# Performance work log

Hardware: AMD Instinct MI355X
Metric: run time of the kernel (lower is better)

Reference implementation:

```python
import jax, jax.numpy as jnp
import numpy as np

N_NODES = 20000
N_EDGES = 240000
N_GRAPHS = 200
D_IN = 118
H = 256          # simplified hidden width standing in for the mul=50 irreps hidden
NB = 10          # number_of_basis
RH = 100         # fc_neurons hidden
L = 3            # layers
SH = 9           # lmax=2 -> 1+3+5 spherical-harmonic channels
MAX_RADIUS = 5.0
NUM_NEIGHBORS = 12.0


def setup_inputs() -> dict:
    key = jax.random.key(0)
    ks = jax.random.split(key, 16)
    inp = {
        "x": jax.random.normal(ks[0], (N_NODES, D_IN), jnp.float32),
        "pos": jax.random.normal(ks[1], (N_NODES, 3), jnp.float32),
        "edge_shift": jax.random.normal(ks[2], (N_EDGES, 3), jnp.float32),
        "lattice": jax.random.normal(ks[3], (N_GRAPHS, 3, 3), jnp.float32),
        "W_embed": jax.random.normal(ks[4], (D_IN, H), jnp.float32) / np.sqrt(D_IN),
        "r1": jax.random.normal(ks[5], (L, NB, RH), jnp.float32) / np.sqrt(NB),
        "b1": jax.random.normal(ks[6], (L, RH), jnp.float32) * 0.1,
        "r2": jax.random.normal(ks[7], (L, RH, H), jnp.float32) / np.sqrt(RH),
        "Wtp": jax.random.normal(ks[8], (L, SH, H, H), jnp.float32) / np.sqrt(SH * H),
        "Wself": jax.random.normal(ks[9], (L, H, H), jnp.float32) / np.sqrt(H),
        "Wskip": jax.random.normal(ks[10], (L, H, H), jnp.float32) / np.sqrt(H),
        "Wout": jax.random.normal(ks[11], (H, 1), jnp.float32) / np.sqrt(H),
        "edge_index": jax.random.randint(ks[12], (2, N_EDGES), 0, N_NODES, jnp.int64)
                        if jax.config.jax_enable_x64 else
                      jax.random.randint(ks[12], (2, N_EDGES), 0, N_NODES).astype(jnp.int32),
        "batch": jnp.sort(jax.random.randint(ks[13], (N_NODES,), 0, N_GRAPHS)).astype(jnp.int32),
    }
    return inp


def _sph_harm_lmax2(u):
    """Component-normalized real spherical harmonics up to l=2 on unit vectors u [E,3]."""
    x, y, z = u[:, 0], u[:, 1], u[:, 2]
    c1 = np.sqrt(3.0)
    c2 = np.sqrt(15.0)
    return jnp.stack([
        jnp.ones_like(x),                       # l=0
        c1 * x, c1 * y, c1 * z,                 # l=1
        c2 * x * y, c2 * y * z,                 # l=2
        (np.sqrt(5.0) / 2.0) * (3.0 * z * z - 1.0),
        c2 * x * z, (c2 / 2.0) * (x * x - y * y),
    ], axis=1)                                  # [E, 9]


def _soft_one_hot_cosine(lens):
    """e3nn soft_one_hot_linspace(basis='cosine', cutoff=True) * sqrt(NB)."""
    vals = jnp.linspace(0.0, MAX_RADIUS, NB + 2)
    step = vals[1] - vals[0]
    vals = vals[1:-1]
    diff = (lens[:, None] - vals[None, :]) / step          # [E, NB]
    emb = jnp.cos(0.5 * jnp.pi * diff) * (diff > -1.0) * (diff < 1.0)
    return emb * np.sqrt(float(NB))


def _forward(x, pos, edge_shift, lattice, W_embed, r1, b1, r2, Wtp, Wself, Wskip, Wout,
             edge_src, edge_dst, batch):
    edge_batch = batch[edge_src]                            # [E]
    # periodic edge vectors: pos[dst] - pos[src] + shift @ lattice[graph]
    edge_vec = pos[edge_dst] - pos[edge_src] + jnp.einsum(
        'ni,nij->nj', edge_shift, lattice[edge_batch])      # [E, 3]
    lens = jnp.linalg.norm(edge_vec, axis=1)                # [E]
    u = edge_vec / (lens[:, None] + 1e-12)
    sh = _sph_harm_lmax2(u)                                 # [E, 9]
    emb = _soft_one_hot_cosine(lens)                        # [E, NB]

    h = x @ W_embed                                         # [N, H]
    inv_sqrt_deg = 1.0 / np.sqrt(NUM_NEIGHBORS)
    for l in range(L):
        radial = jax.nn.silu(emb @ r1[l] + b1[l]) @ r2[l]   # [E, H]
        hs = h[edge_src] * radial                           # gather + radial gate
        # weighted tensor-product-like message: sum_a (hs * sh_a) @ Wtp[l, a]
        msg = (hs * sh[:, 0:1]) @ Wtp[l, 0]
        for a in range(1, SH):
            msg = msg + (hs * sh[:, a:a + 1]) @ Wtp[l, a]   # [E, H]
        agg = jax.ops.segment_sum(msg, edge_dst, num_segments=N_NODES) * inv_sqrt_deg
        h = jax.nn.gelu(agg @ Wself[l] + h @ Wskip[l])      # [N, H]

    node_out = h @ Wout                                     # [N, 1]
    # scatter_mean over graphs
    sums = jax.ops.segment_sum(node_out, batch, num_segments=N_GRAPHS)
    cnts = jax.ops.segment_sum(jnp.ones((N_NODES, 1), node_out.dtype), batch,
                               num_segments=N_GRAPHS)
    return sums / jnp.maximum(cnts, 1.0)                    # [G, 1]


def reference(x, pos, edge_shift, lattice, W_embed, r1, b1, r2, Wtp, Wself, Wskip, Wout,
              edge_index, batch):
    return _forward(x, pos, edge_shift, lattice, W_embed, r1, b1, r2, Wtp, Wself, Wskip,
                    Wout, edge_index[0], edge_index[1], batch)
```

## Files before the change

### kernel.cpp

```cpp
#include <hip/hip_runtime.h>
#include <hip/hip_bf16.h>
#include <cstddef>
#include <cstdint>

#define NNODE  20000
#define MPAD   20096
#define NEDGE  240000
#define NGRAPH 200
#define DIN    118
#define HD     256
#define NBASIS 10
#define RHID   100
#define NLAYER 3
#define NSH    9
#define SHSTR  16
#define KTP    (NSH * HD)
#define KTOT   (KTP + HD)
#define KR2    128
#define KEMB   128
#define SPLITK 4
#define KCH    (KTOT / SPLITK)
#define NRT    (MPAD / 64)

typedef _Float16 f16;
typedef _Float16 f16x2 __attribute__((ext_vector_type(2)));
typedef _Float16 f16x4 __attribute__((ext_vector_type(4)));
typedef _Float16 f16x8 __attribute__((ext_vector_type(8)));
typedef float    f32x4 __attribute__((ext_vector_type(4)));

__device__ __forceinline__ float gelu_tanh(float v) {
  float v3 = v * v * v;
  return 0.5f * v * (1.f + tanhf(0.7978845608028654f * (v + 0.044715f * v3)));
}

__device__ __forceinline__ int perm64(int rho) {
  return (rho & ~63) | ((rho & 15) * 4 + ((rho >> 4) & 3));
}
__device__ __forceinline__ int inv_perm64(int n) {
  return (n & ~63) | (((n & 3) << 4) | ((n >> 2) & 15));
}

__global__ void deg_hist_kernel(const int* __restrict__ ei, int* __restrict__ deg)
{
  int e = blockIdx.x * 256 + threadIdx.x;
  if (e >= NEDGE) return;
  atomicAdd(&deg[ei[NEDGE + e]], 1);
}

__global__ void scan_kernel(const int* __restrict__ deg, int* __restrict__ rowptr)
{
  __shared__ int part[256];
  int t = threadIdx.x;
  const int chunk = (NNODE + 255) / 256;
  int start = t * chunk;
  int end = min(start + chunk, NNODE);
  int s = 0;
  for (int i = start; i < end; ++i) s += deg[i];
  part[t] = s;
  __syncthreads();
  for (int off = 1; off < 256; off <<= 1) {
    int v = (t >= off) ? part[t - off] : 0;
    __syncthreads();
    part[t] += v;
    __syncthreads();
  }
  int run = (t == 0) ? 0 : part[t - 1];
  for (int i = start; i < end; ++i) { rowptr[i] = run; run += deg[i]; }
  if (t == 255) rowptr[NNODE] = run;
}

__global__ void edge_geom_kernel(const float* __restrict__ pos,
                                 const float* __restrict__ shift,
                                 const float* __restrict__ lat,
                                 const int* __restrict__ ei,
                                 const int* __restrict__ batch,
                                 const int* __restrict__ rowptr,
                                 int* __restrict__ cursor,
                                 f16* __restrict__ sh_s,
                                 float* __restrict__ lens_s)
{
  int e = blockIdx.x * 256 + threadIdx.x;
  if (e >= NEDGE) return;
  int src = ei[e];
  int dst = ei[NEDGE + e];
  int b = batch[src];
  const float* L = lat + (size_t)b * 9;
  float s0 = shift[e * 3 + 0], s1 = shift[e * 3 + 1], s2 = shift[e * 3 + 2];
  float ev[3];
#pragma unroll
  for (int j = 0; j < 3; ++j)
    ev[j] = pos[dst * 3 + j] - pos[src * 3 + j] + s0 * L[j] + s1 * L[3 + j] + s2 * L[6 + j];
  float len = sqrtf(ev[0] * ev[0] + ev[1] * ev[1] + ev[2] * ev[2]);
  float inv = 1.f / (len + 1e-12f);
  float x = ev[0] * inv, y = ev[1] * inv, z = ev[2] * inv;
  const float c1 = 1.7320508075688772f;
  const float c2 = 3.872983346207417f;
  int p = atomicAdd(&cursor[dst], 1);
  int si = rowptr[dst] + p;
  f16* she = sh_s + (size_t)si * SHSTR;
  she[0] = (f16)1.f;
  she[1] = (f16)(c1 * x);
  she[2] = (f16)(c1 * y);
  she[3] = (f16)(c1 * z);
  she[4] = (f16)(c2 * x * y);
  she[5] = (f16)(c2 * y * z);
  she[6] = (f16)(1.1180339887498949f * (3.f * z * z - 1.f));
  she[7] = (f16)(c2 * x * z);
  she[8] = (f16)(1.9364916731037085f * (x * x - y * y));
  she[9] = (f16)0.f;
  *(int*)(she + 10) = src;
  she[12] = (f16)0.f; she[13] = (f16)0.f; she[14] = (f16)0.f; she[15] = (f16)0.f;
  lens_s[si] = len;
}

__global__ void prep_kernel(const float* __restrict__ Wtp_l,
                            const float* __restrict__ Wself_l,
                            const float* __restrict__ Wskip_l,
                            const float* __restrict__ r2l,
                            const float* __restrict__ r1l,
                            const float* __restrict__ b1l,
                            f16* __restrict__ Wtp16,
                            f16* __restrict__ WselfT16,
                            f16* __restrict__ Bcat,
                            f16* __restrict__ r2h,
                            f16* __restrict__ r1h)
{
  int b = blockIdx.x, t = threadIdx.x;
  if (b < KTP) {
    int i = b * 256 + t;
    Wtp16[i] = (f16)Wtp_l[i];
  } else if (b < KTP + 256) {
    int n = b - KTP;
    WselfT16[(size_t)n * HD + t] = (f16)(Wself_l[(size_t)t * HD + n] * 0.28867513459481287f);
  } else if (b < KTP + 512) {
    int rho = b - KTP - 256;
    int pcol = perm64(rho);
    Bcat[(size_t)rho * KTOT + KTP + t] = (f16)Wskip_l[(size_t)t * HD + pcol];
  } else if (b < KTP + 768) {
    int rho = b - KTP - 512;
    if (t < KR2) {
      int p = perm64(rho);
      r2h[(size_t)rho * KR2 + t] = (t < RHID) ? (f16)r2l[(size_t)t * HD + p] : (f16)0.f;
    }
  } else {
#pragma unroll
    for (int u = 0; u < 16; ++u) {
      int idx = u * 256 + t;
      int n = idx >> 5, j = idx & 31;
      float v = 0.f;
      if (n < RHID) {
        if (j < NBASIS) v = r1l[(size_t)j * RHID + n];
        else if (j == NBASIS) v = b1l[n];
      }
      r1h[idx] = (f16)v;
    }
  }
}

__global__ void convert_x_kernel(const float* __restrict__ x, f16* __restrict__ xh)
{
  int i = blockIdx.x * 2 + (threadIdx.x >> 7);
  int k = threadIdx.x & 127;
  xh[(size_t)i * KEMB + k] = (i < NNODE && k < DIN) ? (f16)x[(size_t)i * DIN + k] : (f16)0.f;
}

__global__ void convert_wemb_kernel(const float* __restrict__ Wemb, f16* __restrict__ WembT16)
{
  int n = blockIdx.x, k = threadIdx.x;
  WembT16[(size_t)n * KEMB + k] = (k < DIN) ? (f16)Wemb[(size_t)k * HD + n] : (f16)0.f;
}

__global__ __launch_bounds__(256) void gemm_nt_kernel(
    const f16* __restrict__ A, const f16* __restrict__ B,
    f16* __restrict__ C, int K, int ldc, int permRows)
{
  __shared__ __align__(16) f16 As[4][64][8];
  __shared__ __align__(16) f16 Bs[4][128][8];
  int t = threadIdx.x;
  int lane = t & 63, w = t >> 6;
  int row0 = blockIdx.x * 64;
  int n0 = blockIdx.y * 128;
  f32x4 acc[2][4];
#pragma unroll
  for (int i = 0; i < 2; ++i)
#pragma unroll
    for (int j = 0; j < 4; ++j) acc[i][j] = (f32x4){0.f, 0.f, 0.f, 0.f};
  int mq = (w & 1) * 32, nq = (w >> 1) * 64;
  for (int k0 = 0; k0 < K; k0 += 32) {
    {
      int row = t & 63, cc = t >> 6;
      *(uint4*)&As[cc][row][0] = *(const uint4*)(A + (size_t)(row0 + row) * K + k0 + cc * 8);
    }
#pragma unroll
    for (int u = 0; u < 2; ++u) {
      int idx = t + u * 256;
      int ch = idx >> 7, nn = idx & 127;
      *(uint4*)&Bs[ch][nn][0] = *(const uint4*)(B + (size_t)(n0 + nn) * K + k0 + ch * 8);
    }
    __syncthreads();
    int q = lane >> 4, r = lane & 15;
    f16x8 af[2], bfr[4];
#pragma unroll
    for (int i = 0; i < 2; ++i) af[i] = *(const f16x8*)&As[q][mq + i * 16 + r][0];
#pragma unroll
    for (int j = 0; j < 4; ++j) bfr[j] = *(const f16x8*)&Bs[q][nq + j * 16 + r][0];
#pragma unroll
    for (int i = 0; i < 2; ++i)
#pragma unroll
      for (int j = 0; j < 4; ++j)
        acc[i][j] = __builtin_amdgcn_mfma_f32_16x16x32_f16(af[i], bfr[j], acc[i][j], 0, 0, 0);
    __syncthreads();
  }
  int q4 = ((lane >> 4)) * 4, cl = lane & 15;
#pragma unroll
  for (int i = 0; i < 2; ++i)
#pragma unroll
    for (int rr = 0; rr < 4; ++rr) {
      int row = row0 + mq + i * 16 + q4 + rr;
      int orow = permRows ? inv_perm64(row) : row;
#pragma unroll
      for (int j = 0; j < 4; ++j)
        C[(size_t)orow * ldc + n0 + nq + j * 16 + cl] = (f16)acc[i][j][rr];
    }
}

#define RHSTR 136
__global__ __launch_bounds__(256) void radial_kernel(
    const float* __restrict__ lens_s,
    const f16* __restrict__ r1h,
    const f16* __restrict__ r2h,
    f16* __restrict__ rad)
{
  __shared__ __align__(16) f16 emb_s[64][40];
  __shared__ __align__(16) f16 rhA[64 * RHSTR];
  int t = threadIdx.x;
  int lane = t & 63, w = t >> 6;
  int r = lane & 15, q = lane >> 4;
  int e0 = blockIdx.x * 64;

  {
    float len = lens_s[e0 + lane];
    const float step = 5.f / 11.f;
    const float sq = 3.1622776601683795f;
    f16x8 v;
#pragma unroll
    for (int kk = 0; kk < 8; ++kk) {
      int j = w * 8 + kk;
      float val = 0.f;
      if (j < NBASIS) {
        float d = (len - (float)(j + 1) * step) / step;
        val = (d > -1.f && d < 1.f) ? (__cosf(1.5707963267948966f * d) * sq) : 0.f;
      } else if (j == NBASIS) {
        val = 1.f;
      }
      v[kk] = (f16)val;
    }
    *(f16x8*)&emb_s[lane][w * 8] = v;
  }

  int n0w = w * 64;
  f16x8 bfr[4][4];
#pragma unroll
  for (int j = 0; j < 4; ++j)
#pragma unroll
    for (int ks = 0; ks < 4; ++ks)
      bfr[j][ks] = *(const f16x8*)(r2h + (size_t)(n0w + j * 16 + r) * KR2 + ks * 32 + q * 8);

  f16x8 b1f[2];
#pragma unroll
  for (int j = 0; j < 2; ++j)
    b1f[j] = *(const f16x8*)(r1h + (size_t)((2 * w + j) * 16 + r) * 32 + q * 8);

  __syncthreads();

  f32x4 acc1[4][2];
#pragma unroll
  for (int i = 0; i < 4; ++i)
#pragma unroll
    for (int j = 0; j < 2; ++j) acc1[i][j] = (f32x4){0.f, 0.f, 0.f, 0.f};
  {
    f16x8 a1f[4];
#pragma unroll
    for (int i = 0; i < 4; ++i)
      a1f[i] = *(const f16x8*)&emb_s[i * 16 + r][q * 8];
#pragma unroll
    for (int i = 0; i < 4; ++i)
#pragma unroll
      for (int j = 0; j < 2; ++j)
        acc1[i][j] = __builtin_amdgcn_mfma_f32_16x16x32_f16(a1f[i], b1f[j], acc1[i][j], 0, 0, 0);
  }

#pragma unroll
  for (int i = 0; i < 4; ++i)
#pragma unroll
    for (int j = 0; j < 2; ++j)
#pragma unroll
      for (int rr = 0; rr < 4; ++rr) {
        float s = acc1[i][j][rr];
        s = __fdividef(s, 1.f + __expf(-s));
        rhA[(i * 16 + q * 4 + rr) * RHSTR + (2 * w + j) * 16 + r] = (f16)s;
      }
  __syncthreads();

  f32x4 acc[4][4];
#pragma unroll
  for (int i = 0; i < 4; ++i)
#pragma unroll
    for (int j = 0; j < 4; ++j) acc[i][j] = (f32x4){0.f, 0.f, 0.f, 0.f};
#pragma unroll
  for (int ks = 0; ks < 4; ++ks) {
    f16x8 af[4];
#pragma unroll
    for (int i = 0; i < 4; ++i)
      af[i] = *(const f16x8*)&rhA[(i * 16 + r) * RHSTR + ks * 32 + q * 8];
#pragma unroll
    for (int i = 0; i < 4; ++i)
#pragma unroll
      for (int j = 0; j < 4; ++j)
        acc[i][j] = __builtin_amdgcn_mfma_f32_16x16x32_f16(af[i], bfr[j][ks], acc[i][j], 0, 0, 0);
  }

#pragma unroll
  for (int i = 0; i < 4; ++i)
#pragma unroll
    for (int rr = 0; rr < 4; ++rr) {
      int m = i * 16 + q * 4 + rr;
      f16x4 o;
#pragma unroll
      for (int j = 0; j < 4; ++j) o[j] = (f16)acc[i][j][rr];
      *(f16x4*)(rad + (size_t)(e0 + m) * HD + n0w + r * 4) = o;
    }
}

__global__ __launch_bounds__(256) void gather2_kernel(
    const int* __restrict__ rowptr, const f16* __restrict__ rad,
    const f16* __restrict__ h, const f16* __restrict__ sh_s,
    f16* __restrict__ T)
{
  int t = threadIdx.x;
  int half = t >> 7, lc = t & 127;
  int base = blockIdx.x * 4;
  for (int s = 0; s < 2; ++s) {
    int n = base + s * 2 + half;
    int beg = rowptr[n], end = rowptr[n + 1];
    float a0[NSH], a1[NSH];
#pragma unroll
    for (int a = 0; a < NSH; ++a) { a0[a] = 0.f; a1[a] = 0.f; }
    int j = beg;
    for (; j + 2 <= end; j += 2) {
      const f16* she0 = sh_s + (size_t)j * SHSTR;
      const f16* she1 = she0 + SHSTR;
      f16x8 s80 = *(const f16x8*)she0;
      f16x8 s81 = *(const f16x8*)she1;
      float s8v0 = (float)she0[8];
      float s8v1 = (float)she1[8];
      int src0 = *(const int*)(she0 + 10);
      int src1 = *(const int*)(she1 + 10);
      f16x2 rv0 = *(const f16x2*)(rad + (size_t)j * HD + 2 * lc);
      f16x2 rv1 = *(const f16x2*)(rad + (size_t)(j + 1) * HD + 2 * lc);
      f16x2 hv0 = *(const f16x2*)(h + (size_t)src0 * HD + 2 * lc);
      f16x2 hv1 = *(const f16x2*)(h + (size_t)src1 * HD + 2 * lc);
      float p00 = (float)rv0[0] * (float)hv0[0];
      float p01 = (float)rv0[1] * (float)hv0[1];
      float p10 = (float)rv1[0] * (float)hv1[0];
      float p11 = (float)rv1[1] * (float)hv1[1];
#pragma unroll
      for (int a = 0; a < 8; ++a) {
        float sv0 = (float)s80[a], sv1 = (float)s81[a];
        a0[a] += sv0 * p00 + sv1 * p10;
        a1[a] += sv0 * p01 + sv1 * p11;
      }
      a0[8] += s8v0 * p00 + s8v1 * p10;
      a1[8] += s8v0 * p01 + s8v1 * p11;
    }
    if (j < end) {
      const f16* she = sh_s + (size_t)j * SHSTR;
      f16x8 s8 = *(const f16x8*)she;
      float s8v = (float)she[8];
      int src = *(const int*)(she + 10);
      f16x2 rv = *(const f16x2*)(rad + (size_t)j * HD + 2 * lc);
      f16x2 hv = *(const f16x2*)(h + (size_t)src * HD + 2 * lc);
      float p0 = (float)rv[0] * (float)hv[0];
      float p1 = (float)rv[1] * (float)hv[1];
#pragma unroll
      for (int a = 0; a < 8; ++a) {
        float sv = (float)s8[a];
        a0[a] += sv * p0; a1[a] += sv * p1;
      }
      a0[8] += s8v * p0; a1[8] += s8v * p1;
    }
    f16* Tn = T + (size_t)n * KTP + 2 * lc;
#pragma unroll
    for (int a = 0; a < NSH; ++a) {
      f16x2 o; o[0] = (f16)a0[a]; o[1] = (f16)a1[a];
      *(f16x2*)(Tn + a * HD) = o;
    }
  }
}

#define GBM 64
#define GBN 128
__global__ __launch_bounds__(256) void gemm_splitk_kernel(
    const f16* __restrict__ A1,
    const f16* __restrict__ A2,
    const f16* __restrict__ B,
    float* __restrict__ P)
{
  __shared__ __align__(16) f16 As[4][GBM][8];
  __shared__ __align__(16) f16 Bs[4][GBN][8];
  int t = threadIdx.x;
  int lane = t & 63, w = t >> 6;
  int kc = blockIdx.x;
  int row0 = blockIdx.y * GBM;
  int n0 = blockIdx.z * GBN;
  f32x4 acc[2][4];
#pragma unroll
  for (int i = 0; i < 2; ++i)
#pragma unroll
    for (int j = 0; j < 4; ++j) acc[i][j] = (f32x4){0.f, 0.f, 0.f, 0.f};
  int mq = (w & 1) * 32, nq = (w >> 1) * 64;
  int kbeg = kc * KCH;
  int arow = t >> 2, acc4 = t & 3;

  for (int k0 = kbeg; k0 < kbeg + KCH; k0 += 32) {
    {
      const f16* ga = (k0 < KTP)
          ? (A1 + (size_t)(row0 + arow) * KTP + k0 + acc4 * 8)
          : (A2 + (size_t)(row0 + arow) * HD + (k0 - KTP) + acc4 * 8);
      *(uint4*)&As[acc4][arow][0] = *(const uint4*)ga;
    }
#pragma unroll
    for (int u = 0; u < 2; ++u) {
      int idx = t + u * 256;
      int nn = idx >> 2, ch = idx & 3;
      *(uint4*)&Bs[ch][nn][0] = *(const uint4*)(B + (size_t)(n0 + nn) * KTOT + k0 + ch * 8);
    }
    __syncthreads();
    int q = lane >> 4, r = lane & 15;
    f16x8 af[2], bfr[4];
#pragma unroll
    for (int i = 0; i < 2; ++i) af[i] = *(const f16x8*)&As[q][mq + i * 16 + r][0];
#pragma unroll
    for (int j = 0; j < 4; ++j) bfr[j] = *(const f16x8*)&Bs[q][nq + j * 16 + r][0];
#pragma unroll
    for (int i = 0; i < 2; ++i)
#pragma unroll
      for (int j = 0; j < 4; ++j)
        acc[i][j] = __builtin_amdgcn_mfma_f32_16x16x32_f16(af[i], bfr[j], acc[i][j], 0, 0, 0);
    __syncthreads();
  }
  float* Pb = P + ((size_t)(blockIdx.z * NRT + blockIdx.y) * SPLITK + kc) * 8192;
#pragma unroll
  for (int i = 0; i < 2; ++i)
#pragma unroll
    for (int j = 0; j < 4; ++j)
      *(f32x4*)(Pb + (i * 4 + j) * 1024 + t * 4) = acc[i][j];
}

__global__ __launch_bounds__(256) void reduce_kernel(const float* __restrict__ P,
                                                     f16* __restrict__ C)
{
  int t = threadIdx.x;
  int row0 = blockIdx.x * GBM;
  int n0 = blockIdx.y * GBN;
  const float* Pb = P + ((size_t)(blockIdx.y * NRT + blockIdx.x) * SPLITK) * 8192;
  f32x4 s[8];
#pragma unroll
  for (int sl = 0; sl < 8; ++sl) {
    f32x4 v = *(const f32x4*)(Pb + sl * 1024 + t * 4);
#pragma unroll
    for (int kc = 1; kc < SPLITK; ++kc)
      v += *(const f32x4*)(Pb + kc * 8192 + sl * 1024 + t * 4);
    s[sl] = v;
  }
  int lane = t & 63, w = t >> 6;
  int mq = (w & 1) * 32, nq = (w >> 1) * 64;
  int q4 = (lane >> 4) * 4, cl = lane & 15;
#pragma unroll
  for (int i = 0; i < 2; ++i)
#pragma unroll
    for (int rr = 0; rr < 4; ++rr) {
      int row = row0 + mq + i * 16 + q4 + rr;
      f16x4 o;
#pragma unroll
      for (int j = 0; j < 4; ++j) o[j] = (f16)gelu_tanh(s[i * 4 + j][rr]);
      *(f16x4*)(C + (size_t)row * HD + n0 + nq + cl * 4) = o;
    }
}

__global__ __launch_bounds__(256) void node_out_fused_kernel(
    const f16* __restrict__ h,
    const float* __restrict__ Wout,
    const int* __restrict__ batch,
    float* __restrict__ out)
{
  __shared__ float red[256];
  int g = blockIdx.x;
  int t = threadIdx.x;
  int lo = 0, hi = NNODE;
  while (lo < hi) { int mid = (lo + hi) >> 1; if (batch[mid] < g) lo = mid + 1; else hi = mid; }
  int start = lo;
  hi = NNODE;
  while (lo < hi) { int mid = (lo + hi) >> 1; if (batch[mid] < g + 1) lo = mid + 1; else hi = mid; }
  int end = lo;
  int half = t >> 7, lc = t & 127;
  float a0 = 0.f, a1 = 0.f;
  for (int n = start + half; n < end; n += 2) {
    f16x2 v = *(const f16x2*)(h + (size_t)n * HD + 2 * lc);
    a0 += (float)v[0];
    a1 += (float)v[1];
  }
  red[t] = a0 * Wout[2 * lc] + a1 * Wout[2 * lc + 1];
  for (int off = 128; off > 0; off >>= 1) {
    __syncthreads();
    if (t < off) red[t] += red[t + off];
  }
  if (t == 0) out[g] = red[0] / fmaxf((float)(end - start), 1.f);
}

extern "C" void kernel_launch(void* const* d_in, const int* in_sizes, int n_in,
                              void* d_out, int out_size, void* d_ws, size_t ws_size,
                              hipStream_t stream)
{
  (void)in_sizes; (void)n_in; (void)out_size;
  const float* x     = (const float*)d_in[0];
  const float* pos   = (const float*)d_in[1];
  const float* shift = (const float*)d_in[2];
  const float* lat   = (const float*)d_in[3];
  const float* Wemb  = (const float*)d_in[4];
  const float* r1    = (const float*)d_in[5];
  const float* b1    = (const float*)d_in[6];
  const float* r2    = (const float*)d_in[7];
  const float* Wtp   = (const float*)d_in[8];
  const float* Wself = (const float*)d_in[9];
  const float* Wskip = (const float*)d_in[10];
  const float* Wout  = (const float*)d_in[11];
  const int*   eidx  = (const int*)d_in[12];
  const int*   batch = (const int*)d_in[13];
  float* out = (float*)d_out;

  char* ws = (char*)d_ws;
  size_t off = 0;
  auto alloc = [&](size_t bytes) -> char* {
    char* p = ws + off;
    off += (bytes + 255) & ~(size_t)255;
    return p;
  };
  f16*   sh_s    = (f16*)alloc((size_t)NEDGE * SHSTR * 2);
  float* lens_s  = (float*)alloc((size_t)NEDGE * 4);
  f16*   hA      = (f16*)alloc((size_t)MPAD * HD * 2);
  f16*   hB      = (f16*)alloc((size_t)MPAD * HD * 2);
  f16*   T       = (f16*)alloc((size_t)MPAD * KTP * 2);
  f16*   rad     = (f16*)alloc((size_t)NEDGE * HD * 2);
  f16*   Bcat    = (f16*)alloc((size_t)HD * KTOT * 2);
  f16*   r2h     = (f16*)alloc((size_t)HD * KR2 * 2);
  f16*   r1hb    = (f16*)alloc((size_t)128 * 32 * 2);
  f16*   Wtp16   = (f16*)alloc((size_t)KTP * HD * 2);
  f16*   WselfT16= (f16*)alloc((size_t)HD * HD * 2);
  int*   rowptr  = (int*)alloc((size_t)(NNODE + 1) * 4);
  int*   deg     = (int*)alloc((size_t)NNODE * 4);
  int*   cursor  = (int*)alloc((size_t)NNODE * 4);
  if (off > ws_size) return;

  f16*   xh      = rad;
  f16*   WembT16 = rad + (size_t)MPAD * KEMB;
  float* P       = (float*)rad;

  hipMemsetAsync(deg, 0, (size_t)NNODE * 4, stream);
  hipMemsetAsync(cursor, 0, (size_t)NNODE * 4, stream);

  const int EB = (NEDGE + 255) / 256;
  deg_hist_kernel<<<EB, 256, 0, stream>>>(eidx, deg);
  scan_kernel<<<1, 256, 0, stream>>>(deg, rowptr);
  edge_geom_kernel<<<EB, 256, 0, stream>>>(pos, shift, lat, eidx, batch,
                                           rowptr, cursor, sh_s, lens_s);

  convert_x_kernel<<<MPAD / 2, 256, 0, stream>>>(x, xh);
  convert_wemb_kernel<<<HD, KEMB, 0, stream>>>(Wemb, WembT16);
  {
    dim3 eg(MPAD / 64, HD / 128);
    gemm_nt_kernel<<<eg, 256, 0, stream>>>(xh, WembT16, hA, KEMB, HD, 0);
  }

  f16* hcur = hA;
  f16* hnxt = hB;
  dim3 ggrid(SPLITK, NRT, 2);
  dim3 rgrid(NRT, 2);
  dim3 wgrid(HD / 64, KTP / 128);
  for (int l = 0; l < NLAYER; ++l) {
    const float* r1l = r1 + (size_t)l * NBASIS * RHID;
    const float* b1l = b1 + (size_t)l * RHID;
    const float* r2l = r2 + (size_t)l * RHID * HD;
    const float* Wtp_l = Wtp + (size_t)l * NSH * HD * HD;
    const float* Wself_l = Wself + (size_t)l * HD * HD;
    const float* Wskip_l = Wskip + (size_t)l * HD * HD;

    prep_kernel<<<KTP + 768 + 1, 256, 0, stream>>>(Wtp_l, Wself_l, Wskip_l, r2l,
                                                   r1l, b1l,
                                                   Wtp16, WselfT16, Bcat, r2h, r1hb);
    gemm_nt_kernel<<<wgrid, 256, 0, stream>>>(WselfT16, Wtp16, Bcat, HD, KTOT, 1);

    radial_kernel<<<NEDGE / 64, 256, 0, stream>>>(lens_s, r1hb, r2h, rad);
    gather2_kernel<<<NNODE / 4, 256, 0, stream>>>(rowptr, rad, hcur, sh_s, T);
    gemm_splitk_kernel<<<ggrid, 256, 0, stream>>>(T, hcur, Bcat, P);
    reduce_kernel<<<rgrid, 2 * 0 + 256, 0, stream>>>(P, hnxt);
    f16* tmp = hcur; hcur = hnxt; hnxt = tmp;
  }

  node_out_fused_kernel<<<NGRAPH, 256, 0, stream>>>(hcur, Wout, batch, out);
}
```

Baseline: 755.1 us.

## Replace split-K GEMM plus reduce with double-buffered fused GEMM using direct-to-LDS loads

The split-K node GEMM and its separate reduce/GELU kernel are merged into one kernel that walks the full K dimension per tile and applies GELU in its epilogue. Global-to-LDS copies now use global_load_lds into a double-buffered shared tile, so the next K step loads while the current one runs MFMA. This removes the fp32 partial-sum round trip through memory and one launch per layer. The cost is a grid four times smaller (314x2 blocks), which may leave CUs underused, plus a longer serial K loop per block.

```diff
diff --git a/kernel.cpp b/kernel.cpp
--- a/kernel.cpp
+++ b/kernel.cpp
@@ -18,8 +18,6 @@
 #define KTOT   (KTP + HD)
 #define KR2    128
 #define KEMB   128
-#define SPLITK 4
-#define KCH    (KTOT / SPLITK)
 #define NRT    (MPAD / 64)
 
 typedef _Float16 f16;
@@ -31,6 +29,12 @@
 __device__ __forceinline__ float gelu_tanh(float v) {
   float v3 = v * v * v;
   return 0.5f * v * (1.f + tanhf(0.7978845608028654f * (v + 0.044715f * v3)));
+}
+
+__device__ __forceinline__ void gload16(const void* g, void* l) {
+  __builtin_amdgcn_global_load_lds(
+      (const __attribute__((address_space(1))) unsigned int*)g,
+      (__attribute__((address_space(3))) unsigned int*)l, 16, 0, 0);
 }
 
 __device__ __forceinline__ int perm64(int rho) {
@@ -400,81 +404,62 @@
 
 #define GBM 64
 #define GBN 128
-__global__ __launch_bounds__(256) void gemm_splitk_kernel(
+#define NKSTEP (KTOT / 32)
+__global__ __launch_bounds__(256) void gemm_fused_kernel(
     const f16* __restrict__ A1,
     const f16* __restrict__ A2,
     const f16* __restrict__ B,
-    float* __restrict__ P)
-{
-  __shared__ __align__(16) f16 As[4][GBM][8];
-  __shared__ __align__(16) f16 Bs[4][GBN][8];
+    f16* __restrict__ C)
+{
+  __shared__ __align__(16) f16 As[2][GBM][4][8];
+  __shared__ __align__(16) f16 Bs[2][GBN][4][8];
   int t = threadIdx.x;
   int lane = t & 63, w = t >> 6;
-  int kc = blockIdx.x;
-  int row0 = blockIdx.y * GBM;
-  int n0 = blockIdx.z * GBN;
+  int row0 = blockIdx.x * GBM;
+  int n0 = blockIdx.y * GBN;
+  int mq = (w & 1) * 32, nq = (w >> 1) * 64;
+  int arow = t >> 2, ach = t & 3;
+
   f32x4 acc[2][4];
 #pragma unroll
   for (int i = 0; i < 2; ++i)
 #pragma unroll
     for (int j = 0; j < 4; ++j) acc[i][j] = (f32x4){0.f, 0.f, 0.f, 0.f};
-  int mq = (w & 1) * 32, nq = (w >> 1) * 64;
-  int kbeg = kc * KCH;
-  int arow = t >> 2, acc4 = t & 3;
-
-  for (int k0 = kbeg; k0 < kbeg + KCH; k0 += 32) {
-    {
-      const f16* ga = (k0 < KTP)
-          ? (A1 + (size_t)(row0 + arow) * KTP + k0 + acc4 * 8)
-          : (A2 + (size_t)(row0 + arow) * HD + (k0 - KTP) + acc4 * 8);
-      *(uint4*)&As[acc4][arow][0] = *(const uint4*)ga;
-    }
+
+  auto stage = [&](int buf, int k0) {
+    const f16* ga = (k0 < KTP)
+        ? (A1 + (size_t)(row0 + arow) * KTP + k0 + ach * 8)
+        : (A2 + (size_t)(row0 + arow) * HD + (k0 - KTP) + ach * 8);
+    gload16(ga, &As[buf][0][0][0] + (size_t)w * 512);
 #pragma unroll
     for (int u = 0; u < 2; ++u) {
       int idx = t + u * 256;
-      int nn = idx >> 2, ch = idx & 3;
-      *(uint4*)&Bs[ch][nn][0] = *(const uint4*)(B + (size_t)(n0 + nn) * KTOT + k0 + ch * 8);
-    }
-    __syncthreads();
-    int q = lane >> 4, r = lane & 15;
+      const f16* gb = B + (size_t)(n0 + (idx >> 2)) * KTOT + k0 + (idx & 3) * 8;
+      gload16(gb, &Bs[buf][0][0][0] + (size_t)(u * 256 + w * 64) * 8);
+    }
+  };
+
+  stage(0, 0);
+  __syncthreads();
+
+  int cur = 0;
+  int q = lane >> 4, r = lane & 15;
+  for (int s = 0; s < NKSTEP; ++s) {
+    if (s + 1 < NKSTEP) stage(cur ^ 1, (s + 1) * 32);
     f16x8 af[2], bfr[4];
 #pragma unroll
-    for (int i = 0; i < 2; ++i) af[i] = *(const f16x8*)&As[q][mq + i * 16 + r][0];
-#pragma unroll
-    for (int j = 0; j < 4; ++j) bfr[j] = *(const f16x8*)&Bs[q][nq + j * 16 + r][0];
+    for (int i = 0; i < 2; ++i) af[i] = *(const f16x8*)&As[cur][mq + i * 16 + r][q][0];
+#pragma unroll
+    for (int j = 0; j < 4; ++j) bfr[j] = *(const f16x8*)&Bs[cur][nq + j * 16 + r][q][0];
 #pragma unroll
     for (int i = 0; i < 2; ++i)
 #pragma unroll
       for (int j = 0; j < 4; ++j)
         acc[i][j] = __builtin_amdgcn_mfma_f32_16x16x32_f16(af[i], bfr[j], acc[i][j], 0, 0, 0);
     __syncthreads();
-  }
-  float* Pb = P + ((size_t)(blockIdx.z * NRT + blockIdx.y) * SPLITK + kc) * 8192;
-#pragma unroll
-  for (int i = 0; i < 2; ++i)
-#pragma unroll
-    for (int j = 0; j < 4; ++j)
-      *(f32x4*)(Pb + (i * 4 + j) * 1024 + t * 4) = acc[i][j];
-}
-
-__global__ __launch_bounds__(256) void reduce_kernel(const float* __restrict__ P,
-                                                     f16* __restrict__ C)
-{
-  int t = threadIdx.x;
-  int row0 = blockIdx.x * GBM;
-  int n0 = blockIdx.y * GBN;
-  const float* Pb = P + ((size_t)(blockIdx.y * NRT + blockIdx.x) * SPLITK) * 8192;
-  f32x4 s[8];
-#pragma unroll
-  for (int sl = 0; sl < 8; ++sl) {
-    f32x4 v = *(const f32x4*)(Pb + sl * 1024 + t * 4);
-#pragma unroll
-    for (int kc = 1; kc < SPLITK; ++kc)
-      v += *(const f32x4*)(Pb + kc * 8192 + sl * 1024 + t * 4);
-    s[sl] = v;
-  }
-  int lane = t & 63, w = t >> 6;
-  int mq = (w & 1) * 32, nq = (w >> 1) * 64;
+    cur ^= 1;
+  }
+
   int q4 = (lane >> 4) * 4, cl = lane & 15;
 #pragma unroll
   for (int i = 0; i < 2; ++i)
@@ -483,7 +468,7 @@
       int row = row0 + mq + i * 16 + q4 + rr;
       f16x4 o;
 #pragma unroll
-      for (int j = 0; j < 4; ++j) o[j] = (f16)gelu_tanh(s[i * 4 + j][rr]);
+      for (int j = 0; j < 4; ++j) o[j] = (f16)gelu_tanh(acc[i][j][rr]);
       *(f16x4*)(C + (size_t)row * HD + n0 + nq + cl * 4) = o;
     }
 }
@@ -564,7 +549,6 @@
 
   f16*   xh      = rad;
   f16*   WembT16 = rad + (size_t)MPAD * KEMB;
-  float* P       = (float*)rad;
 
   hipMemsetAsync(deg, 0, (size_t)NNODE * 4, stream);
   hipMemsetAsync(cursor, 0, (size_t)NNODE * 4, stream);
@@ -584,8 +568,7 @@
 
   f16* hcur = hA;
   f16* hnxt = hB;
-  dim3 ggrid(SPLITK, NRT, 2);
-  dim3 rgrid(NRT, 2);
+  dim3 fgrid(NRT, 2);
   dim3 wgrid(HD / 64, KTP / 128);
   for (int l = 0; l < NLAYER; ++l) {
     const float* r1l = r1 + (size_t)l * NBASIS * RHID;
@@ -602,8 +585,7 @@
 
     radial_kernel<<<NEDGE / 64, 256, 0, stream>>>(lens_s, r1hb, r2h, rad);
     gather2_kernel<<<NNODE / 4, 256, 0, stream>>>(rowptr, rad, hcur, sh_s, T);
-    gemm_splitk_kernel<<<ggrid, 256, 0, stream>>>(T, hcur, Bcat, P);
-    reduce_kernel<<<rgrid, 2 * 0 + 256, 0, stream>>>(P, hnxt);
+    gemm_fused_kernel<<<fgrid, 256, 0, stream>>>(T, hcur, Bcat, hnxt);
     f16* tmp = hcur; hcur = hnxt; hnxt = tmp;
   }
 
```

Result: faster. 721.1 us (-4.5%).
